# Kernel tuning notes

Hardware: AMD Instinct MI355X
Metric: run time of the kernel (lower is better)

## Reference

```python
import jax, jax.numpy as jnp
import numpy as np

N, E = 50000, 800000
F_IN, EDGE_DIM, H, C = 128, 64, 8, 32
NEG_SLOPE = 0.2


def setup_inputs() -> dict:
    key = jax.random.key(0)
    ks = jax.random.split(key, 9)
    return {
        "x": jax.random.normal(ks[0], (N, F_IN), dtype=jnp.float32),
        "edge_index": jax.random.randint(ks[1], (2, E), 0, N, dtype=jnp.int32),
        "edge_attr": jax.random.normal(ks[2], (E, EDGE_DIM), dtype=jnp.float32),
        "W": jax.random.normal(ks[3], (F_IN, H * C), dtype=jnp.float32) * 0.05,
        "att_src": jax.random.normal(ks[4], (H, C), dtype=jnp.float32) * 0.05,
        "att_dst": jax.random.normal(ks[5], (H, C), dtype=jnp.float32) * 0.05,
        "W_edge": jax.random.normal(ks[6], (EDGE_DIM, H * C), dtype=jnp.float32) * 0.05,
        "att_edge": jax.random.normal(ks[7], (H, C), dtype=jnp.float32) * 0.05,
        "bias": jax.random.normal(ks[8], (H * C,), dtype=jnp.float32) * 0.05,
    }


def reference(x, edge_index, edge_attr, W, att_src, att_dst, W_edge, att_edge, bias):
    src, dst = edge_index[0], edge_index[1]  # messages flow src -> dst
    # Pre-activation ReLU from Graph_intra.forward
    xr = jax.nn.relu(x)
    # Linear projection, per-head view: [N, H, C]
    xs = (xr @ W).reshape(N, H, C)
    # Per-node attention logits: [N, H]
    a_src = jnp.einsum("nhc,hc->nh", xs, att_src)
    a_dst = jnp.einsum("nhc,hc->nh", xs, att_dst)
    # Edge-feature attention contribution: [E, H]
    e_proj = (edge_attr @ W_edge).reshape(E, H, C)
    a_edge = jnp.einsum("ehc,hc->eh", e_proj, att_edge)
    # Per-edge logits + LeakyReLU
    alpha = jax.nn.leaky_relu(a_src[src] + a_dst[dst] + a_edge, NEG_SLOPE)  # [E, H]
    # Segment softmax over destination neighborhoods
    seg_max = jax.ops.segment_max(alpha, dst, num_segments=N)
    seg_max = jnp.where(jnp.isfinite(seg_max), seg_max, 0.0)
    alpha = jnp.exp(alpha - seg_max[dst])
    seg_sum = jax.ops.segment_sum(alpha, dst, num_segments=N)
    alpha = alpha / (seg_sum[dst] + 1e-16)
    # Weighted message aggregation: scatter-add alpha_e * x_src[e]
    msgs = alpha[:, :, None] * xs[src]  # [E, H, C]
    out = jax.ops.segment_sum(msgs, dst, num_segments=N)  # [N, H, C]
    return out.reshape(N, H * C) + bias
```

## Files before the change

kernel.cpp:

```cpp
#include <hip/hip_runtime.h>

#define N_NODES 50000
#define E_EDGES 800000
#define F_IN    128
#define EDGE_DIM 64
#define HC      256
#define NEG_SLOPE 0.2f

typedef __attribute__((ext_vector_type(8))) short short8;
typedef __attribute__((ext_vector_type(4))) float f32x4;

__device__ __forceinline__ unsigned short f2bf(float f) {
    unsigned u = __builtin_bit_cast(unsigned, f);
    u += 0x7fffu + ((u >> 16) & 1u);
    return (unsigned short)(u >> 16);
}
__device__ __forceinline__ float bf2f(unsigned short b) {
    return __builtin_bit_cast(float, (unsigned)b << 16);
}

__global__ __launch_bounds__(256) void k_pre(const float* __restrict__ W,
        const float* __restrict__ att_src, const float* __restrict__ att_dst,
        const float* __restrict__ W_edge, const float* __restrict__ att_edge,
        unsigned short* __restrict__ W_T, unsigned short* __restrict__ WaT,
        unsigned short* __restrict__ WaE, int* __restrict__ counts, int* __restrict__ gcur) {
    int idx = blockIdx.x * 256 + threadIdx.x;
    if (idx < N_NODES) counts[idx] = 0;
    if (idx == 0) *gcur = 0;
    if (idx < 32768) {
        int n = idx >> 7, k = idx & 127;
        W_T[n * 128 + k] = f2bf(W[k * 256 + n]);
    }
    if (idx < 2048) {
        int col = idx & 15, k = idx >> 4;
        const float* att = (col < 8) ? att_src : att_dst;
        int h = col & 7;
        float s = 0.f;
        #pragma unroll
        for (int c = 0; c < 32; ++c)
            s = fmaf(W[k * 256 + h * 32 + c], att[h * 32 + c], s);
        WaT[col * 128 + k] = f2bf(s);
    }
    if (idx < 1024) {
        int c = idx >> 6, k = idx & 63;
        float s = 0.f;
        if (c < 8) {
            #pragma unroll
            for (int cc = 0; cc < 32; ++cc)
                s = fmaf(W_edge[k * 256 + c * 32 + cc], att_edge[c * 32 + cc], s);
        }
        WaE[c * 64 + k] = (c < 8) ? f2bf(s) : (unsigned short)0;
    }
}

#define HIST_BLOCKS 782
#define ALOG_BLOCKS 782
__global__ __launch_bounds__(256) void kA(const float* __restrict__ x,
        const unsigned short* __restrict__ WaT,
        const int4* __restrict__ dst4, int* __restrict__ counts, int4* __restrict__ slot4,
        float* __restrict__ a_src, float* __restrict__ a_dst) {
    int t = threadIdx.x;
    if (blockIdx.x < HIST_BLOCKS) {
        int i = blockIdx.x * 256 + t;
        if (i < E_EDGES / 4) {
            int4 d = dst4[i];
            int4 sl;
            sl.x = atomicAdd(&counts[d.x], 1);
            sl.y = atomicAdd(&counts[d.y], 1);
            sl.z = atomicAdd(&counts[d.z], 1);
            sl.w = atomicAdd(&counts[d.w], 1);
            slot4[i] = sl;
        }
        return;
    }
    int tile = (blockIdx.x - HIST_BLOCKS) * 4 + (t >> 6);
    if (tile >= N_NODES / 16) return;
    int lane = t & 63, mr = lane & 15, g = lane >> 4;
    int node = tile * 16 + mr;
    f32x4 acc = (f32x4){0.f, 0.f, 0.f, 0.f};
    #pragma unroll
    for (int ks = 0; ks < 4; ++ks) {
        const float* xp = &x[(size_t)node * 128 + ks * 32 + g * 8];
        short8 a;
        #pragma unroll
        for (int j = 0; j < 8; ++j) a[j] = (short)f2bf(fmaxf(xp[j], 0.f));
        short8 b = *(const short8*)&WaT[mr * 128 + ks * 32 + g * 8];
        acc = __builtin_amdgcn_mfma_f32_16x16x32_bf16(a, b, acc, 0, 0, 0);
    }
    #pragma unroll
    for (int r = 0; r < 4; ++r) {
        int n2 = tile * 16 + g * 4 + r;
        if (mr < 8) a_src[n2 * 8 + mr]       = acc[r];
        else        a_dst[n2 * 8 + (mr - 8)] = acc[r];
    }
}

__global__ __launch_bounds__(256) void kB_alloc(const int* __restrict__ counts,
                                                int* __restrict__ starts,
                                                int* __restrict__ gcur) {
    int n = blockIdx.x * 256 + threadIdx.x;
    int c = (n < N_NODES) ? counts[n] : 0;
    int incl = c;
    #pragma unroll
    for (int off = 1; off < 64; off <<= 1) {
        int u = __shfl_up(incl, off);
        if ((threadIdx.x & 63) >= off) incl += u;
    }
    int total = __shfl(incl, 63);
    int wavebase = 0;
    if ((threadIdx.x & 63) == 63) wavebase = atomicAdd(gcur, total);
    wavebase = __shfl(wavebase, 63);
    if (n < N_NODES) starts[n] = wavebase + incl - c;
}

#define NT_TILES 782
#define K1_GRID 512
__global__ __launch_bounds__(256, 2) void kC(const float* __restrict__ x,
        const unsigned short* __restrict__ W_T, const unsigned short* __restrict__ WaE,
        const float* __restrict__ ea,
        const int* __restrict__ src, const int* __restrict__ dst,
        const int* __restrict__ slot, const int* __restrict__ starts,
        const float* __restrict__ a_src, const float* __restrict__ a_dst,
        unsigned short* __restrict__ xs,
        _Float16* __restrict__ w_perm, int* __restrict__ src_perm) {
    __shared__ __align__(16) char smem[81920];
    int t = threadIdx.x;

    if (blockIdx.x >= K1_GRID) {
        int* s_sn  = (int*)smem;
        int* s_dn  = (int*)(smem + 1024);
        int* s_pos = (int*)(smem + 2048);
        int blockbase = (blockIdx.x - K1_GRID) * 256;
        {
            int e = blockbase + t;
            int dn = dst[e], sn = src[e];
            int pos = starts[dn] + slot[e];
            s_sn[t] = sn; s_dn[t] = dn; s_pos[t] = pos;
            src_perm[pos] = sn;
        }
        __syncthreads();
        int lane = t & 63, w = t >> 6;
        int mr = lane & 15, g = lane >> 4;
        short8 b0 = *(const short8*)&WaE[mr * 64 + g * 8];
        short8 b1 = *(const short8*)&WaE[mr * 64 + 32 + g * 8];
        #pragma unroll
        for (int ti = 0; ti < 4; ++ti) {
            int lb = w * 64 + ti * 16;
            int er = blockbase + lb + mr;
            const float* ap = &ea[(size_t)er * 64 + g * 8];
            short8 a0, a1;
            #pragma unroll
            for (int j = 0; j < 8; ++j) a0[j] = (short)f2bf(ap[j]);
            #pragma unroll
            for (int j = 0; j < 8; ++j) a1[j] = (short)f2bf(ap[32 + j]);
            f32x4 acc = (f32x4){0.f, 0.f, 0.f, 0.f};
            acc = __builtin_amdgcn_mfma_f32_16x16x32_bf16(a0, b0, acc, 0, 0, 0);
            acc = __builtin_amdgcn_mfma_f32_16x16x32_bf16(a1, b1, acc, 0, 0, 0);
            if (mr < 8) {
                #pragma unroll
                for (int r = 0; r < 4; ++r) {
                    int le = lb + g * 4 + r;
                    int sn = s_sn[le], dn = s_dn[le];
                    float v = acc[r] + a_src[sn * 8 + mr] + a_dst[dn * 8 + mr];
                    v = (v > 0.f) ? v : NEG_SLOPE * v;
                    w_perm[(size_t)s_pos[le] * 8 + mr] = (_Float16)__expf(v);
                }
            }
        }
        return;
    }

    unsigned short* sB = (unsigned short*)smem;
    unsigned short* sA = (unsigned short*)(smem + 65536);
    for (int G = t; G < 4096; G += 256) {
        int n = G >> 4, gi = G & 15;
        *(int4*)&sB[(n * 16 + (gi ^ (n & 7))) * 8] = *(const int4*)&W_T[n * 128 + gi * 8];
    }
    int lane = t & 63, w = t >> 6, mr = lane & 15, g = lane >> 4;

    bool first = true;
    for (int rt = blockIdx.x; rt < NT_TILES; rt += K1_GRID) {
        if (!first) __syncthreads();
        first = false;
        for (int G = t; G < 1024; G += 256) {
            int r = G >> 4, gi = G & 15;
            int node = rt * 64 + r;
            unsigned short pk[8];
            if (node < N_NODES) {
                const float* xp = &x[(long)node * 128 + gi * 8];
                #pragma unroll
                for (int jj = 0; jj < 8; ++jj) pk[jj] = f2bf(fmaxf(xp[jj], 0.f));
            } else {
                #pragma unroll
                for (int jj = 0; jj < 8; ++jj) pk[jj] = 0;
            }
            *(int4*)&sA[(r * 16 + (gi ^ (r & 7))) * 8] = *(int4*)pk;
        }
        __syncthreads();

        f32x4 acc[16];
        #pragma unroll
        for (int i = 0; i < 16; ++i) acc[i] = (f32x4){0.f, 0.f, 0.f, 0.f};

        int r16 = w * 16 + mr;
        #pragma unroll
        for (int ks = 0; ks < 4; ++ks) {
            int pos = (ks * 4 + g) ^ (mr & 7);
            short8 a = *(const short8*)&sA[(r16 * 16 + pos) * 8];
            #pragma unroll
            for (int nt = 0; nt < 16; ++nt) {
                short8 b = *(const short8*)&sB[((nt * 16 + mr) * 16 + pos) * 8];
                acc[nt] = __builtin_amdgcn_mfma_f32_16x16x32_bf16(a, b, acc[nt], 0, 0, 0);
            }
        }

        #pragma unroll
        for (int r = 0; r < 4; ++r) {
            int node = rt * 64 + w * 16 + g * 4 + r;
            if (node < N_NODES) {
                #pragma unroll
                for (int nt = 0; nt < 16; ++nt)
                    xs[(long)node * 256 + nt * 16 + mr] = f2bf(acc[nt][r]);
            }
        }
    }
}

__global__ __launch_bounds__(256) void k6_wave(
    const int* __restrict__ starts, const int* __restrict__ counts,
    const _Float16* __restrict__ w_perm, const int* __restrict__ src_perm,
    const unsigned short* __restrict__ xs, const float* __restrict__ bias,
    float* __restrict__ out) {
    int lane = threadIdx.x & 63;
    int n = blockIdx.x * 4 + (threadIdx.x >> 6);
    if (n >= N_NODES) return;
    int start = starts[n], cnt = counts[n];
    int j = lane >> 3;
    int hq = lane >> 3;

    float acc0 = 0.f, acc1 = 0.f, acc2 = 0.f, acc3 = 0.f;
    float psum = 0.f;
    for (int base = 0; base < cnt; base += 8) {
        int nk = cnt - base; if (nk > 8) nk = 8;
        float wv = (float)w_perm[(size_t)(start + base) * 8 + lane];
        if (j >= nk) wv = 0.f;
        psum += wv;
        int sv = src_perm[start + base + (lane & 7)];
        #pragma unroll
        for (int jj = 0; jj < 8; ++jj) {
            int s = __shfl(sv, jj);
            s = (jj < nk) ? s : 0;
            float w = __shfl(wv, jj * 8 + hq);
            ushort4 xv = *(const ushort4*)&xs[(size_t)s * 256 + lane * 4];
            acc0 = fmaf(w, bf2f(xv.x), acc0);
            acc1 = fmaf(w, bf2f(xv.y), acc1);
            acc2 = fmaf(w, bf2f(xv.z), acc2);
            acc3 = fmaf(w, bf2f(xv.w), acc3);
        }
    }
    psum += __shfl_xor(psum, 8);
    psum += __shfl_xor(psum, 16);
    psum += __shfl_xor(psum, 32);
    float denom = __shfl(psum, hq);
    float rinv = 1.0f / (denom + 1e-16f);
    float4 bv = *(const float4*)&bias[lane * 4];
    f32x4 o;
    o[0] = acc0 * rinv + bv.x;
    o[1] = acc1 * rinv + bv.y;
    o[2] = acc2 * rinv + bv.z;
    o[3] = acc3 * rinv + bv.w;
    __builtin_nontemporal_store(o, (f32x4*)&out[(size_t)n * 256 + lane * 4]);
}

extern "C" void kernel_launch(void* const* d_in, const int* in_sizes, int n_in,
                              void* d_out, int out_size, void* d_ws, size_t ws_size,
                              hipStream_t stream) {
    const float* x         = (const float*)d_in[0];
    const int*   ei        = (const int*)d_in[1];
    const float* edge_attr = (const float*)d_in[2];
    const float* W         = (const float*)d_in[3];
    const float* att_src   = (const float*)d_in[4];
    const float* att_dst   = (const float*)d_in[5];
    const float* W_edge    = (const float*)d_in[6];
    const float* att_edge  = (const float*)d_in[7];
    const float* bias      = (const float*)d_in[8];
    float* out = (float*)d_out;

    const int* e_src = ei;
    const int* e_dst = ei + E_EDGES;

    char* p = (char*)d_ws;
    unsigned short* xs = (unsigned short*)p; p += (size_t)N_NODES * HC * 2;
    float* a_src   = (float*)p; p += (size_t)N_NODES * 8 * 4;
    float* a_dst   = (float*)p; p += (size_t)N_NODES * 8 * 4;
    _Float16* w_perm = (_Float16*)p; p += (size_t)E_EDGES * 8 * 2 + 256;
    int* src_perm  = (int*)p;   p += (size_t)E_EDGES * 4 + 256;
    int* slot      = (int*)p;   p += (size_t)E_EDGES * 4 + 256;
    unsigned short* W_T  = (unsigned short*)p; p += 32768 * 2;
    unsigned short* WaT  = (unsigned short*)p; p += 2048 * 2;
    unsigned short* WaE  = (unsigned short*)p; p += 1024 * 2;
    int* counts    = (int*)p;   p += 200192;
    int* starts    = (int*)p;   p += 200192;
    int* gcur      = (int*)p;   p += 256;

    hipLaunchKernelGGL(k_pre, dim3(196), dim3(256), 0, stream,
                       W, att_src, att_dst, W_edge, att_edge, W_T, WaT, WaE, counts, gcur);
    hipLaunchKernelGGL(kA, dim3(HIST_BLOCKS + ALOG_BLOCKS), dim3(256), 0, stream,
                       x, WaT, (const int4*)e_dst, counts, (int4*)slot, a_src, a_dst);
    hipLaunchKernelGGL(kB_alloc, dim3(196), dim3(256), 0, stream,
                       counts, starts, gcur);
    hipLaunchKernelGGL(kC, dim3(K1_GRID + E_EDGES / 256), dim3(256), 0, stream,
                       x, W_T, WaE, edge_attr, e_src, e_dst, slot, starts,
                       a_src, a_dst, xs, w_perm, src_perm);
    hipLaunchKernelGGL(k6_wave, dim3(N_NODES / 4), dim3(256), 0, stream,
                       starts, counts, w_perm, src_perm, xs, bias, out);
}
```

Measured before the change: 211.2 us.

## Split node GEMM across output-column halves and load A fragments directly to registers

The node projection GEMM in kC now gives each block one 128-column half of W, so shared memory drops from 80KB to 32KB and more blocks can be resident per CU. The x tile is no longer staged through LDS: each lane loads its relu'd bf16 A fragments straight from global memory into registers, which removes a barrier per tile. The tradeoff is that x is read twice, once per column half, and the per-lane global loads are strided and less coalesced. The launch-bounds occupancy hint is also dropped.

```diff
diff --git a/kernel.cpp b/kernel.cpp
--- a/kernel.cpp
+++ b/kernel.cpp
@@ -114,8 +114,8 @@
 }
 
 #define NT_TILES 782
-#define K1_GRID 512
-__global__ __launch_bounds__(256, 2) void kC(const float* __restrict__ x,
+#define GEMM_BLOCKS 512
+__global__ __launch_bounds__(256) void kC(const float* __restrict__ x,
         const unsigned short* __restrict__ W_T, const unsigned short* __restrict__ WaE,
         const float* __restrict__ ea,
         const int* __restrict__ src, const int* __restrict__ dst,
@@ -123,14 +123,14 @@
         const float* __restrict__ a_src, const float* __restrict__ a_dst,
         unsigned short* __restrict__ xs,
         _Float16* __restrict__ w_perm, int* __restrict__ src_perm) {
-    __shared__ __align__(16) char smem[81920];
+    __shared__ __align__(16) char smem[32768];
     int t = threadIdx.x;
 
-    if (blockIdx.x >= K1_GRID) {
+    if (blockIdx.x >= GEMM_BLOCKS) {
         int* s_sn  = (int*)smem;
         int* s_dn  = (int*)(smem + 1024);
         int* s_pos = (int*)(smem + 2048);
-        int blockbase = (blockIdx.x - K1_GRID) * 256;
+        int blockbase = (blockIdx.x - GEMM_BLOCKS) * 256;
         {
             int e = blockbase + t;
             int dn = dst[e], sn = src[e];
@@ -171,56 +171,54 @@
     }
 
     unsigned short* sB = (unsigned short*)smem;
-    unsigned short* sA = (unsigned short*)(smem + 65536);
-    for (int G = t; G < 4096; G += 256) {
-        int n = G >> 4, gi = G & 15;
-        *(int4*)&sB[(n * 16 + (gi ^ (n & 7))) * 8] = *(const int4*)&W_T[n * 128 + gi * 8];
-    }
+    int ch = blockIdx.x >> 8;
+    int rt0 = blockIdx.x & 255;
+    for (int G = t; G < 2048; G += 256) {
+        int nn = G >> 4, gi = G & 15;
+        *(int4*)&sB[(nn * 16 + (gi ^ (nn & 7))) * 8] =
+            *(const int4*)&W_T[(ch * 128 + nn) * 128 + gi * 8];
+    }
+    __syncthreads();
     int lane = t & 63, w = t >> 6, mr = lane & 15, g = lane >> 4;
 
-    bool first = true;
-    for (int rt = blockIdx.x; rt < NT_TILES; rt += K1_GRID) {
-        if (!first) __syncthreads();
-        first = false;
-        for (int G = t; G < 1024; G += 256) {
-            int r = G >> 4, gi = G & 15;
-            int node = rt * 64 + r;
-            unsigned short pk[8];
-            if (node < N_NODES) {
-                const float* xp = &x[(long)node * 128 + gi * 8];
+    for (int rt = rt0; rt < NT_TILES; rt += 256) {
+        int node = rt * 64 + w * 16 + mr;
+        short8 a[4];
+        if (node < N_NODES) {
+            #pragma unroll
+            for (int ks = 0; ks < 4; ++ks) {
+                const float* xp = &x[(size_t)node * 128 + ks * 32 + g * 8];
                 #pragma unroll
-                for (int jj = 0; jj < 8; ++jj) pk[jj] = f2bf(fmaxf(xp[jj], 0.f));
-            } else {
+                for (int j = 0; j < 8; ++j) a[ks][j] = (short)f2bf(fmaxf(xp[j], 0.f));
+            }
+        } else {
+            #pragma unroll
+            for (int ks = 0; ks < 4; ++ks)
                 #pragma unroll
-                for (int jj = 0; jj < 8; ++jj) pk[jj] = 0;
-            }
-            *(int4*)&sA[(r * 16 + (gi ^ (r & 7))) * 8] = *(int4*)pk;
-        }
-        __syncthreads();
-
-        f32x4 acc[16];
-        #pragma unroll
-        for (int i = 0; i < 16; ++i) acc[i] = (f32x4){0.f, 0.f, 0.f, 0.f};
-
-        int r16 = w * 16 + mr;
+                for (int j = 0; j < 8; ++j) a[ks][j] = 0;
+        }
+
+        f32x4 acc[8];
+        #pragma unroll
+        for (int i = 0; i < 8; ++i) acc[i] = (f32x4){0.f, 0.f, 0.f, 0.f};
+
         #pragma unroll
         for (int ks = 0; ks < 4; ++ks) {
             int pos = (ks * 4 + g) ^ (mr & 7);
-            short8 a = *(const short8*)&sA[(r16 * 16 + pos) * 8];
-            #pragma unroll
-            for (int nt = 0; nt < 16; ++nt) {
+            #pragma unroll
+            for (int nt = 0; nt < 8; ++nt) {
                 short8 b = *(const short8*)&sB[((nt * 16 + mr) * 16 + pos) * 8];
-                acc[nt] = __builtin_amdgcn_mfma_f32_16x16x32_bf16(a, b, acc[nt], 0, 0, 0);
+                acc[nt] = __builtin_amdgcn_mfma_f32_16x16x32_bf16(a[ks], b, acc[nt], 0, 0, 0);
             }
         }
 
         #pragma unroll
         for (int r = 0; r < 4; ++r) {
-            int node = rt * 64 + w * 16 + g * 4 + r;
-            if (node < N_NODES) {
+            int node2 = rt * 64 + w * 16 + g * 4 + r;
+            if (node2 < N_NODES) {
                 #pragma unroll
-                for (int nt = 0; nt < 16; ++nt)
-                    xs[(long)node * 256 + nt * 16 + mr] = f2bf(acc[nt][r]);
+                for (int nt = 0; nt < 8; ++nt)
+                    xs[(size_t)node2 * 256 + ch * 128 + nt * 16 + mr] = f2bf(acc[nt][r]);
             }
         }
     }
@@ -309,7 +307,7 @@
                        x, WaT, (const int4*)e_dst, counts, (int4*)slot, a_src, a_dst);
     hipLaunchKernelGGL(kB_alloc, dim3(196), dim3(256), 0, stream,
                        counts, starts, gcur);
-    hipLaunchKernelGGL(kC, dim3(K1_GRID + E_EDGES / 256), dim3(256), 0, stream,
+    hipLaunchKernelGGL(kC, dim3(GEMM_BLOCKS + E_EDGES / 256), dim3(256), 0, stream,
                        x, W_T, WaE, edge_attr, e_src, e_dst, slot, starts,
                        a_src, a_dst, xs, w_perm, src_perm);
     hipLaunchKernelGGL(k6_wave, dim3(N_NODES / 4), dim3(256), 0, stream,
```

Result: no change. 209.9 us (-0.6%).
